# Performance work log

Hardware: AMD Instinct MI355X
Metric: run time of the kernel (lower is better)

The kernel has to match this reference:

```python
import jax, jax.numpy as jnp
import numpy as np

N = 40000        # nodes
E = 640000       # edges (avg degree 16)
D = 128          # in_dim = hidden_dim = out_dim (heads=1)
L = 3            # num_layers
BLOCK = 64       # big-bird local window
KEEP_P = 0.1     # probability an out-of-window edge is randomly kept
NEG = -1e9


def _xavier(key, shape):
    lim = np.sqrt(6.0 / (shape[-2] + shape[-1])).astype(np.float32)
    return jax.random.uniform(key, shape, jnp.float32, -lim, lim)


def setup_inputs() -> dict:
    key = jax.random.key(0)
    ks = jax.random.split(key, 11)
    x = jax.random.normal(ks[0], (N, D), jnp.float32)
    edge_index = jax.random.randint(ks[1], (2, E), 0, N, dtype=jnp.int64)
    # stacked per-layer params (all layers are D->D since heads=1)
    Wq = _xavier(ks[2], (L, D, D)); Wk = _xavier(ks[3], (L, D, D))
    Wv = _xavier(ks[4], (L, D, D)); Wo = _xavier(ks[5], (L, D, D))
    bq = jax.random.uniform(ks[6], (L, D), jnp.float32, -0.05, 0.05)
    bk = jax.random.uniform(ks[7], (L, D), jnp.float32, -0.05, 0.05)
    bv = jax.random.uniform(ks[8], (L, D), jnp.float32, -0.05, 0.05)
    bo = jax.random.uniform(ks[9], (L, D), jnp.float32, -0.05, 0.05)
    return {"x": x, "edge_index": edge_index,
            "Wq": Wq, "bq": bq, "Wk": Wk, "bk": bk,
            "Wv": Wv, "bv": bv, "Wo": Wo, "bo": bo}


def _bigbird_layer(h, src, dst, edge_mask, Wq, bq, Wk, bk, Wv, bv, Wo, bo):
    # h: [N, D]; src/dst: [E] int; edge_mask: [E] bool (True -> masked out)
    q = h @ Wq + bq                         # [N, D]
    k = h @ Wk + bk
    v = h @ Wv + bv
    scale = 1.0 / jnp.sqrt(jnp.asarray(D, h.dtype))
    alpha = jnp.sum(q[dst] * k[src], axis=-1) * scale   # [E] edge scores
    alpha = jnp.where(edge_mask, NEG, alpha)
    # segment softmax keyed by destination node
    m = jax.ops.segment_max(alpha, dst, num_segments=N)  # [N]
    e = jnp.exp(alpha - m[dst])                          # [E]
    s = jax.ops.segment_sum(e, dst, num_segments=N)      # [N]
    w = e / s[dst]                                       # [E]
    msg = v[src] * w[:, None]                            # [E, D]
    out = jax.ops.segment_sum(msg, dst, num_segments=N)  # [N, D]
    return out @ Wo + bo


def reference(x, edge_index, Wq, bq, Wk, bk, Wv, bv, Wo, bo):
    src, dst = edge_index[0], edge_index[1]
    local_mask = jnp.abs(src - dst) > BLOCK              # outside local window
    h = x
    for i in range(L):
        rkey = jax.random.fold_in(jax.random.key(42), i)
        rand_mask = jax.random.uniform(rkey, (E,)) > KEEP_P
        edge_mask = local_mask & rand_mask               # big-bird mask
        h = _bigbird_layer(h, src, dst, edge_mask,
                           Wq[i], bq[i], Wk[i], bk[i],
                           Wv[i], bv[i], Wo[i], bo[i])
        if i < L - 1:
            h = jax.nn.relu(h)  # dropout is identity in eval mode
    return h
```

## Files before the change

### kernel.cpp

```cpp
#include <hip/hip_runtime.h>
#include <hip/hip_bf16.h>
#include <stdint.h>
#include <math.h>

#define N_NODES 40000
#define N_EDGES 640000
#define DIM     128
#define NLAYERS 3
#define WINDOW  64
#define SCALE_F 0.08838834764831845f
#define CAP     96

#define CVT_XB   (N_NODES * DIM / 4 / 256)
#define CVT_BB   ((4 * NLAYERS * DIM + 255) / 256)
#define CVT_WB   (64 * 12)
#define CVT_CU   ((N_NODES + 255) / 256)
#define CVT_TOT  (CVT_XB + CVT_BB + CVT_WB + CVT_CU)

#define QKV_BLKS 1875
#define MASK_BLKS ((N_EDGES + 255) / 256)

#define HSTR 136

typedef unsigned int   u32;
typedef unsigned short u16;
typedef unsigned long long u64;
typedef unsigned char  u8;

typedef __attribute__((ext_vector_type(8))) short short8;
typedef __attribute__((ext_vector_type(4))) float f32x4;

__device__ inline float bf2f(u32 lo16) { return __uint_as_float(lo16 << 16); }
__device__ inline u16 f2bf(float f) {
  u32 x = __float_as_uint(f);
  u32 r = (x + 0x7fffu + ((x >> 16) & 1u)) >> 16;
  return (u16)r;
}

__host__ __device__ inline u32 rotl32(u32 v, int r) { return (v << r) | (v >> (32 - r)); }
#define TF_R4(a,b,c,d) \
  x0 += x1; x1 = rotl32(x1,a); x1 ^= x0; \
  x0 += x1; x1 = rotl32(x1,b); x1 ^= x0; \
  x0 += x1; x1 = rotl32(x1,c); x1 ^= x0; \
  x0 += x1; x1 = rotl32(x1,d); x1 ^= x0;

__host__ __device__ inline void tf2x32(u32 k0, u32 k1, u32 x0, u32 x1, u32& o0, u32& o1) {
  u32 ks2 = k0 ^ k1 ^ 0x1BD11BDAu;
  x0 += k0; x1 += k1;
  TF_R4(13,15,26,6);   x0 += k1;  x1 += ks2 + 1u;
  TF_R4(17,29,16,24);  x0 += ks2; x1 += k0  + 2u;
  TF_R4(13,15,26,6);   x0 += k0;  x1 += k1  + 3u;
  TF_R4(17,29,16,24);  x0 += k1;  x1 += ks2 + 4u;
  TF_R4(13,15,26,6);   x0 += ks2; x1 += k0  + 5u;
  o0 = x0; o1 = x1;
}

__device__ inline int ld_src(const int* ei, int e, int i64) {
  return i64 ? ei[2 * (size_t)e] : ei[e];
}
__device__ inline int ld_dst(const int* ei, int e, int i64) {
  return i64 ? ei[2 * ((size_t)N_EDGES + (size_t)e)] : ei[N_EDGES + e];
}

__device__ inline void detect_local(const u32* __restrict__ xw,
                                    const int* __restrict__ ei,
                                    int& fl, int& efl) {
  __shared__ int votes, nz;
  if (threadIdx.x == 0) { votes = 0; nz = 0; }
  __syncthreads();
  u32 w = xw[threadIdx.x * 777 + 13];
  int e = (w >> 7) & 0xFF;
  if (e < 100 || e > 135) atomicAdd(&votes, 1);
  if (ei[threadIdx.x * 5000 + 1] != 0) atomicAdd(&nz, 1);
  __syncthreads();
  fl  = (votes == 0) ? 1 : 0;
  efl = (nz == 0) ? 1 : 0;
}

__global__ void k_cvtall(const void* __restrict__ x, const int* __restrict__ ei,
                         const void* bq, const void* bk, const void* bv, const void* bo,
                         const void* Wq, const void* Wk, const void* Wv, const void* Wo,
                         int* __restrict__ flag, int* __restrict__ eflag,
                         int* __restrict__ cursor,
                         u16* __restrict__ xb, float* __restrict__ biasf,
                         u16* __restrict__ wswz) {
  int b = blockIdx.x;
  int fl, efl;
  detect_local((const u32*)x, ei, fl, efl);
  if (b == 0 && threadIdx.x == 0) { *flag = fl; *eflag = efl; }
  if (b < CVT_XB) {
    int i = b * 256 + threadIdx.x;
    if (fl) {
      ((u64*)xb)[i] = ((const u64*)x)[i];
    } else {
      f32x4 v = ((const f32x4*)x)[i];
      u64 p = (u64)f2bf(v.x) | ((u64)f2bf(v.y) << 16)
            | ((u64)f2bf(v.z) << 32) | ((u64)f2bf(v.w) << 48);
      ((u64*)xb)[i] = p;
    }
  } else if (b < CVT_XB + CVT_BB) {
    int i = (b - CVT_XB) * 256 + threadIdx.x;
    if (i < 4 * NLAYERS * DIM) {
      int which = i / (NLAYERS * DIM), rem = i % (NLAYERS * DIM);
      const void* src = (which == 0) ? bq : (which == 1) ? bk : (which == 2) ? bv : bo;
      biasf[i] = fl ? bf2f(((const u16*)src)[rem]) : ((const float*)src)[rem];
    }
  } else if (b < CVT_XB + CVT_BB + CVT_WB) {
    int bb = b - CVT_XB - CVT_BB;
    int m = bb >> 6;
    int l = m >> 2, t = m & 3;
    const void* base = (t == 0 ? Wq : t == 1 ? Wk : t == 2 ? Wv : Wo);
    int idx = (bb & 63) * 256 + threadIdx.x;
    int k = idx >> 7, n = idx & 127;
    u16 val;
    if (fl) val = ((const u16*)base)[l * DIM * DIM + idx];
    else    val = f2bf(((const float*)base)[l * DIM * DIM + idx]);
    int nf = n >> 4, col = n & 15, kk = k >> 5, hi = (k >> 3) & 3, j = k & 7;
    wswz[m * 16384 + ((nf * 4 + kk) * 64 + hi * 16 + col) * 8 + j] = val;
  } else {
    int i = (b - CVT_XB - CVT_BB - CVT_WB) * 256 + threadIdx.x;
    if (i < N_NODES) cursor[i] = 0;
  }
}

__device__ inline void gemm_frags(const u16* A, int rowBase, int lane, short8 af[4]) {
  const u16* arow = A + (size_t)(rowBase + (lane & 15)) * DIM;
  #pragma unroll
  for (int kk = 0; kk < 4; ++kk)
    af[kk] = *(const short8*)(arow + kk * 32 + (lane >> 4) * 8);
}

__global__ __launch_bounds__(256) void k_qkv0_mask(
    const u16* __restrict__ A, const u16* __restrict__ wswzL,
    const float* __restrict__ biasL,
    u16* __restrict__ qb, u16* __restrict__ kb, u16* __restrict__ vb,
    const int* __restrict__ ei, const int* __restrict__ eflag,
    u16* __restrict__ edst, u32* __restrict__ esrck,
    u32 ka0, u32 ka1, u32 kb0, u32 kb1, u32 kc0, u32 kc1) {
  int b = blockIdx.x;
  if (b < QKV_BLKS) {
    int z = b / 625, bx = b - z * 625;
    const u16* W = wswzL + z * 16384;
    const float* bias = biasL + z * NLAYERS * DIM;
    u16* out = (z == 0) ? qb : (z == 1) ? kb : vb;
    int tid = threadIdx.x, wave = tid >> 6, lane = tid & 63;
    int rowBase = bx * 64 + wave * 16;
    short8 af[4];
    gemm_frags(A, rowBase, lane, af);
    int col = lane & 15, rowOff = (lane >> 4) * 4;
    #pragma unroll
    for (int nf = 0; nf < 8; ++nf) {
      f32x4 acc = {0.f, 0.f, 0.f, 0.f};
      #pragma unroll
      for (int kk = 0; kk < 4; ++kk) {
        short8 bfm = *(const short8*)(W + ((nf * 4 + kk) * 64 + lane) * 8);
        acc = __builtin_amdgcn_mfma_f32_16x16x32_bf16(af[kk], bfm, acc, 0, 0, 0);
      }
      float bv = bias[nf * 16 + col];
      #pragma unroll
      for (int i = 0; i < 4; ++i) {
        float vv = acc[i] + bv;
        size_t oidx = (size_t)(rowBase + rowOff + i) * DIM + nf * 16 + col;
        out[oidx] = f2bf(vv);
      }
    }
  } else {
    int e = (b - QKV_BLKS) * 256 + threadIdx.x;
    if (e >= N_EDGES) return;
    int i64 = *eflag;
    int s = ld_src(ei, e, i64), d = ld_dst(ei, e, i64);
    bool loc = abs(s - d) <= WINDOW;
    u32 keys[6] = {ka0, ka1, kb0, kb1, kc0, kc1};
    u32 kept = 0;
    #pragma unroll
    for (int l = 0; l < 3; ++l) {
      u32 b1, b2;
      tf2x32(keys[2*l], keys[2*l+1], 0u, (u32)e, b1, b2);
      u32 bits = b1 ^ b2;
      float u = __uint_as_float(0x3f800000u | (bits >> 9)) - 1.0f;
      if (loc || (u <= 0.1f)) kept |= (1u << l);
    }
    edst[e]  = (u16)d;
    esrck[e] = (u32)s | (kept << 16);
  }
}

__global__ void k_scatter(const u16* __restrict__ edst, const u32* __restrict__ esrck,
                          int* __restrict__ cursor, u32* __restrict__ csr) {
  int c = blockIdx.x & 7;
  int e = (blockIdx.x >> 3) * 256 + threadIdx.x;
  if (e >= N_EDGES) return;
  int d = edst[e];
  if (((d >> 8) & 7) != c) return;
  u32 sk = esrck[e];
  int pos = atomicAdd(&cursor[d], 1);
  if (pos < CAP) csr[(size_t)d * CAP + pos] = sk;
}

__global__ void k_beacon(float* __restrict__ outf, const int* __restrict__ flag,
                         int ws_bad_mb) {
  if (threadIdx.x != 0 || blockIdx.x != 0) return;
  if (*flag == 1) outf[1] = 1024.0f;
  if (ws_bad_mb)  outf[2] = 4096.0f + (float)ws_bad_mb;
}

__global__ __launch_bounds__(256) void k_gemm_oqkv(
    const u16* __restrict__ A,
    const u16* __restrict__ Wo_swz, const float* __restrict__ bo_f,
    const u16* __restrict__ wswzN, const float* __restrict__ biasN,
    u16* __restrict__ qb, u16* __restrict__ kb, u16* __restrict__ vb) {
  __shared__ u16 hl[64 * HSTR];
  int z = blockIdx.z;
  int tid = threadIdx.x, wave = tid >> 6, lane = tid & 63;
  int rowBase = blockIdx.x * 64 + wave * 16;
  int col = lane & 15, rowOff = (lane >> 4) * 4;
  {
    short8 af[4];
    gemm_frags(A, rowBase, lane, af);
    #pragma unroll
    for (int nf = 0; nf < 8; ++nf) {
      f32x4 acc = {0.f, 0.f, 0.f, 0.f};
      #pragma unroll
      for (int kk = 0; kk < 4; ++kk) {
        short8 bfm = *(const short8*)(Wo_swz + ((nf * 4 + kk) * 64 + lane) * 8);
        acc = __builtin_amdgcn_mfma_f32_16x16x32_bf16(af[kk], bfm, acc, 0, 0, 0);
      }
      float bv = bo_f[nf * 16 + col];
      #pragma unroll
      for (int i = 0; i < 4; ++i) {
        float vv = fmaxf(acc[i] + bv, 0.f);
        hl[(wave * 16 + rowOff + i) * HSTR + nf * 16 + col] = f2bf(vv);
      }
    }
  }
  __syncthreads();
  const u16* W = wswzN + z * 16384;
  const float* bias = biasN + z * NLAYERS * DIM;
  u16* out = (z == 0) ? qb : (z == 1) ? kb : vb;
  short8 af2[4];
  {
    const u16* arow = hl + (size_t)(wave * 16 + (lane & 15)) * HSTR;
    #pragma unroll
    for (int kk = 0; kk < 4; ++kk)
      af2[kk] = *(const short8*)(arow + kk * 32 + (lane >> 4) * 8);
  }
  #pragma unroll
  for (int nf = 0; nf < 8; ++nf) {
    f32x4 acc = {0.f, 0.f, 0.f, 0.f};
    #pragma unroll
    for (int kk = 0; kk < 4; ++kk) {
      short8 bfm = *(const short8*)(W + ((nf * 4 + kk) * 64 + lane) * 8);
      acc = __builtin_amdgcn_mfma_f32_16x16x32_bf16(af2[kk], bfm, acc, 0, 0, 0);
    }
    float bv = bias[nf * 16 + col];
    #pragma unroll
    for (int i = 0; i < 4; ++i) {
      float vv = acc[i] + bv;
      size_t oidx = (size_t)(rowBase + rowOff + i) * DIM + nf * 16 + col;
      out[oidx] = f2bf(vv);
    }
  }
}

__global__ __launch_bounds__(256) void k_gemm_o(
    const u16* __restrict__ A, const u16* __restrict__ W,
    const float* __restrict__ bias,
    void* __restrict__ fout, const int* __restrict__ flag) {
  int tid = threadIdx.x, wave = tid >> 6, lane = tid & 63;
  int rowBase = blockIdx.x * 64 + wave * 16;
  short8 af[4];
  gemm_frags(A, rowBase, lane, af);
  int col = lane & 15, rowOff = (lane >> 4) * 4;
  int bf16out = *flag;
  #pragma unroll
  for (int nf = 0; nf < 8; ++nf) {
    f32x4 acc = {0.f, 0.f, 0.f, 0.f};
    #pragma unroll
    for (int kk = 0; kk < 4; ++kk) {
      short8 bfm = *(const short8*)(W + ((nf * 4 + kk) * 64 + lane) * 8);
      acc = __builtin_amdgcn_mfma_f32_16x16x32_bf16(af[kk], bfm, acc, 0, 0, 0);
    }
    float bv = bias[nf * 16 + col];
    #pragma unroll
    for (int i = 0; i < 4; ++i) {
      float vv = acc[i] + bv;
      size_t oidx = (size_t)(rowBase + rowOff + i) * DIM + nf * 16 + col;
      if (bf16out) ((u16*)fout)[oidx] = f2bf(vv);
      else         ((float*)fout)[oidx] = vv;
    }
  }
}

__global__ __launch_bounds__(256) void k_agg(
    const u16* __restrict__ qb, const u16* __restrict__ kb,
    const u16* __restrict__ vb,
    const int* __restrict__ cursor, const u32* __restrict__ csr,
    int layer, u16* __restrict__ msg) {
  int wid  = blockIdx.x * 4 + (threadIdx.x >> 6);
  int lane = threadIdx.x & 63;
  int deg = cursor[wid];
  if (deg > CAP) deg = CAP;
  size_t beg = (size_t)wid * CAP;
  const u32 keptbit = 1u << (16 + layer);
  float m = -__builtin_inff(), s = 0.f, a0 = 0.f, a1 = 0.f;

  if (deg <= 64) {
    u32 en = (lane < deg) ? csr[beg + lane] : 0u;
    u64 km = __ballot((lane < deg) && (en & keptbit));
    if (!km) {
      for (int base = 0; base < deg; base += 4) {
        int c = deg - base; if (c > 4) c = 4;
        u32 w0 = 0, w1 = 0, w2 = 0, w3 = 0;
        if (c > 0) { int t = __shfl((int)en, base + 0) & 0xffff;
                     w0 = ((const u32*)(vb + (size_t)t * DIM))[lane]; }
        if (c > 1) { int t = __shfl((int)en, base + 1) & 0xffff;
                     w1 = ((const u32*)(vb + (size_t)t * DIM))[lane]; }
        if (c > 2) { int t = __shfl((int)en, base + 2) & 0xffff;
                     w2 = ((const u32*)(vb + (size_t)t * DIM))[lane]; }
        if (c > 3) { int t = __shfl((int)en, base + 3) & 0xffff;
                     w3 = ((const u32*)(vb + (size_t)t * DIM))[lane]; }
        if (c > 0) { a0 += bf2f(w0 & 0xffffu); a1 += bf2f(w0 >> 16); }
        if (c > 1) { a0 += bf2f(w1 & 0xffffu); a1 += bf2f(w1 >> 16); }
        if (c > 2) { a0 += bf2f(w2 & 0xffffu); a1 += bf2f(w2 >> 16); }
        if (c > 3) { a0 += bf2f(w3 & 0xffffu); a1 += bf2f(w3 >> 16); }
      }
      s = (float)deg;
    } else if (!(km & (km - 1))) {
      int i = __ffsll((unsigned long long)km) - 1;
      int src = __shfl((int)en, i) & 0xffff;
      u32 vw = ((const u32*)(vb + (size_t)src * DIM))[lane];
      a0 = bf2f(vw & 0xffffu);
      a1 = bf2f(vw >> 16);
      s = 1.f;
    } else {
      u32 qw = ((const u32*)(qb + (size_t)wid * DIM))[lane];
      float q0 = bf2f(qw & 0xffffu), q1 = bf2f(qw >> 16);
      u64 rem = km;
      int i0 = __ffsll((unsigned long long)rem) - 1; rem &= rem - 1;
      int src0 = __shfl((int)en, i0) & 0xffff;
      u32 kw = ((const u32*)(kb + (size_t)src0 * DIM))[lane];
      u32 vw = ((const u32*)(vb + (size_t)src0 * DIM))[lane];
      while (1) {
        u32 kwc = kw, vwc = vw;
        bool more = (rem != 0);
        if (more) {
          int in = __ffsll((unsigned long long)rem) - 1; rem &= rem - 1;
          int sn = __shfl((int)en, in) & 0xffff;
          kw = ((const u32*)(kb + (size_t)sn * DIM))[lane];
          vw = ((const u32*)(vb + (size_t)sn * DIM))[lane];
        }
        float p = q0 * bf2f(kwc & 0xffffu) + q1 * bf2f(kwc >> 16);
        #pragma unroll
        for (int o = 32; o; o >>= 1) p += __shfl_xor(p, o, 64);
        float alpha = p * SCALE_F;
        float mn = fmaxf(m, alpha);
        float c  = __expf(m - mn);
        float w  = __expf(alpha - mn);
        s  = s * c + w;
        a0 = a0 * c + w * bf2f(vwc & 0xffffu);
        a1 = a1 * c + w * bf2f(vwc >> 16);
        m = mn;
        if (!more) break;
      }
    }
  } else {
    u32 qw = ((const u32*)(qb + (size_t)wid * DIM))[lane];
    float q0 = bf2f(qw & 0xffffu), q1 = bf2f(qw >> 16);
    bool anyKept = false;
    for (int base = 0; base < deg; base += 64) {
      int cnt = min(64, deg - base);
      u32 en = (lane < cnt) ? csr[beg + base + lane] : 0u;
      if (__ballot((lane < cnt) && (en & keptbit))) anyKept = true;
    }
    for (int base = 0; base < deg; base += 64) {
      int cnt = min(64, deg - base);
      u32 en = (lane < cnt) ? csr[beg + base + lane] : 0u;
      if (!anyKept) {
        for (int i = 0; i < cnt; ++i) {
          int src = __shfl((int)en, i) & 0xffff;
          u32 vw = ((const u32*)(vb + (size_t)src * DIM))[lane];
          a0 += bf2f(vw & 0xffffu);
          a1 += bf2f(vw >> 16);
        }
        s += (float)cnt;
      } else {
        u64 km = __ballot((lane < cnt) && (en & keptbit));
        while (km) {
          int i = __ffsll((unsigned long long)km) - 1;
          km &= km - 1;
          int src = __shfl((int)en, i) & 0xffff;
          u32 kw = ((const u32*)(kb + (size_t)src * DIM))[lane];
          u32 vw = ((const u32*)(vb + (size_t)src * DIM))[lane];
          float p = q0 * bf2f(kw & 0xffffu) + q1 * bf2f(kw >> 16);
          #pragma unroll
          for (int o = 32; o; o >>= 1) p += __shfl_xor(p, o, 64);
          float alpha = p * SCALE_F;
          float mn = fmaxf(m, alpha);
          float c  = __expf(m - mn);
          float w  = __expf(alpha - mn);
          s  = s * c + w;
          a0 = a0 * c + w * bf2f(vw & 0xffffu);
          a1 = a1 * c + w * bf2f(vw >> 16);
          m = mn;
        }
      }
    }
  }
  float inv = (s > 0.f) ? 1.f / s : 0.f;
  ((u32*)(msg + (size_t)wid * DIM))[lane] =
      (u32)f2bf(a0 * inv) | ((u32)f2bf(a1 * inv) << 16);
}

extern "C" void kernel_launch(void* const* d_in, const int* in_sizes, int n_in,
                              void* d_out, int out_size, void* d_ws, size_t ws_size,
                              hipStream_t stream) {
  const void* x  = d_in[0];
  const int*  ei = (const int*)d_in[1];
  const void* Wq = d_in[2];
  const void* bq = d_in[3];
  const void* Wk = d_in[4];
  const void* bk = d_in[5];
  const void* Wv = d_in[6];
  const void* bv = d_in[7];
  const void* Wo = d_in[8];
  const void* bo = d_in[9];

  char* ws = (char*)d_ws;
  size_t off = 0;
  auto alloc = [&](size_t bytes) -> void* {
    void* p = ws + off;
    off += (bytes + 255) & ~(size_t)255;
    return p;
  };
  u16*   xb   = (u16*)alloc((size_t)N_NODES * DIM * 2);
  u16*   qb   = (u16*)alloc((size_t)N_NODES * DIM * 2);
  u16*   kb2  = (u16*)alloc((size_t)N_NODES * DIM * 2);
  u16*   vb2  = (u16*)alloc((size_t)N_NODES * DIM * 2);
  u16*   msgb = (u16*)alloc((size_t)N_NODES * DIM * 2);
  u16*   edst  = (u16*)alloc((size_t)N_EDGES * 2);
  u32*   esrck = (u32*)alloc((size_t)N_EDGES * 4);
  int*   cursor    = (int*)alloc((size_t)N_NODES * 4);
  u32*   csr       = (u32*)alloc((size_t)N_NODES * CAP * 4);
  u16*   wswz      = (u16*)alloc((size_t)12 * 16384 * 2);
  float* biasf     = (float*)alloc((size_t)4 * NLAYERS * DIM * 4);
  int*   flag      = (int*)alloc(256);
  int*   eflag     = (int*)alloc(256);
  size_t needed = off;
  int ws_bad_mb = (ws_size < needed) ? (int)(ws_size >> 20) + 1 : 0;
  (void)in_sizes; (void)n_in; (void)out_size;

  u32 lk[6];
  for (int l = 0; l < 3; ++l) {
    u32 o0, o1;
    tf2x32(0u, 42u, 0u, (u32)l, o0, o1);
    lk[2 * l] = o0; lk[2 * l + 1] = o1;
  }

  k_cvtall<<<CVT_TOT, 256, 0, stream>>>(
      x, ei, bq, bk, bv, bo, Wq, Wk, Wv, Wo, flag, eflag, cursor, xb, biasf, wswz);
  k_qkv0_mask<<<QKV_BLKS + MASK_BLKS, 256, 0, stream>>>(
      xb, wswz, biasf, qb, kb2, vb2,
      ei, eflag, edst, esrck, lk[0], lk[1], lk[2], lk[3], lk[4], lk[5]);
  k_scatter<<<8 * ((N_EDGES + 255) / 256), 256, 0, stream>>>(edst, esrck, cursor, csr);

  k_agg<<<N_NODES / 4, 256, 0, stream>>>(qb, kb2, vb2, cursor, csr, 0, msgb);
  for (int l = 0; l < NLAYERS - 1; ++l) {
    k_gemm_oqkv<<<dim3(N_NODES / 64, 1, 3), 256, 0, stream>>>(
        msgb,
        wswz + (size_t)(l * 4 + 3) * 16384, biasf + (size_t)(3 * NLAYERS + l) * DIM,
        wswz + (size_t)((l + 1) * 4) * 16384, biasf + (size_t)(l + 1) * DIM,
        qb, kb2, vb2);
    k_agg<<<N_NODES / 4, 256, 0, stream>>>(qb, kb2, vb2, cursor, csr, l + 1, msgb);
  }
  k_gemm_o<<<N_NODES / 64, 256, 0, stream>>>(
      msgb, wswz + (size_t)(2 * 4 + 3) * 16384,
      biasf + (size_t)(3 * NLAYERS + 2) * DIM, d_out, flag);

  k_beacon<<<1, 64, 0, stream>>>((float*)d_out, flag, ws_bad_mb);
}
```

Measured before the change: 192.4 us.

## Batch four kept edges per online-softmax step and interleave q/k/v GEMM blocks

The multi-kept-edge path of the aggregation kernel now gathers up to four K/V rows at once, runs the four dot-product reductions interleaved, and folds them into the online softmax with a single rescale. This exposes more memory-level parallelism and cuts the serial shuffle-reduction chain. The q/k/v GEMM kernels also map block index to (z = b%3, row tile = b/3), so blocks that share the same A rows run next to each other, which should improve cache reuse of the activations. The cost is more registers in the aggregation kernel and different floating-point summation order.

```diff
diff --git a/kernel.cpp b/kernel.cpp
--- a/kernel.cpp
+++ b/kernel.cpp
@@ -10,6 +10,7 @@
 #define WINDOW  64
 #define SCALE_F 0.08838834764831845f
 #define CAP     96
+#define NEG_INF (-__builtin_inff())
 
 #define CVT_XB   (N_NODES * DIM / 4 / 256)
 #define CVT_BB   ((4 * NLAYERS * DIM + 255) / 256)
@@ -139,7 +140,7 @@
     u32 ka0, u32 ka1, u32 kb0, u32 kb1, u32 kc0, u32 kc1) {
   int b = blockIdx.x;
   if (b < QKV_BLKS) {
-    int z = b / 625, bx = b - z * 625;
+    int z = b % 3, bx = b / 3;
     const u16* W = wswzL + z * 16384;
     const float* bias = biasL + z * NLAYERS * DIM;
     u16* out = (z == 0) ? qb : (z == 1) ? kb : vb;
@@ -210,9 +211,10 @@
     const u16* __restrict__ wswzN, const float* __restrict__ biasN,
     u16* __restrict__ qb, u16* __restrict__ kb, u16* __restrict__ vb) {
   __shared__ u16 hl[64 * HSTR];
-  int z = blockIdx.z;
+  int b = blockIdx.x;
+  int z = b % 3, bx = b / 3;
   int tid = threadIdx.x, wave = tid >> 6, lane = tid & 63;
-  int rowBase = blockIdx.x * 64 + wave * 16;
+  int rowBase = bx * 64 + wave * 16;
   int col = lane & 15, rowOff = (lane >> 4) * 4;
   {
     short8 af[4];
@@ -302,7 +304,7 @@
   if (deg > CAP) deg = CAP;
   size_t beg = (size_t)wid * CAP;
   const u32 keptbit = 1u << (16 + layer);
-  float m = -__builtin_inff(), s = 0.f, a0 = 0.f, a1 = 0.f;
+  float m = NEG_INF, s = 0.f, a0 = 0.f, a1 = 0.f;
 
   if (deg <= 64) {
     u32 en = (lane < deg) ? csr[beg + lane] : 0u;
@@ -336,31 +338,55 @@
       u32 qw = ((const u32*)(qb + (size_t)wid * DIM))[lane];
       float q0 = bf2f(qw & 0xffffu), q1 = bf2f(qw >> 16);
       u64 rem = km;
-      int i0 = __ffsll((unsigned long long)rem) - 1; rem &= rem - 1;
-      int src0 = __shfl((int)en, i0) & 0xffff;
-      u32 kw = ((const u32*)(kb + (size_t)src0 * DIM))[lane];
-      u32 vw = ((const u32*)(vb + (size_t)src0 * DIM))[lane];
-      while (1) {
-        u32 kwc = kw, vwc = vw;
-        bool more = (rem != 0);
-        if (more) {
-          int in = __ffsll((unsigned long long)rem) - 1; rem &= rem - 1;
-          int sn = __shfl((int)en, in) & 0xffff;
-          kw = ((const u32*)(kb + (size_t)sn * DIM))[lane];
-          vw = ((const u32*)(vb + (size_t)sn * DIM))[lane];
+      while (rem) {
+        int n = 1;
+        int j0 = __ffsll((unsigned long long)rem) - 1; rem &= rem - 1;
+        int j1 = 0, j2 = 0, j3 = 0;
+        if (rem) { j1 = __ffsll((unsigned long long)rem) - 1; rem &= rem - 1; n = 2; }
+        if (rem) { j2 = __ffsll((unsigned long long)rem) - 1; rem &= rem - 1; n = 3; }
+        if (rem) { j3 = __ffsll((unsigned long long)rem) - 1; rem &= rem - 1; n = 4; }
+        u32 kw0 = 0, kw1 = 0, kw2 = 0, kw3 = 0;
+        u32 vw0 = 0, vw1 = 0, vw2 = 0, vw3 = 0;
+        {            int t = __shfl((int)en, j0) & 0xffff;
+                     kw0 = ((const u32*)(kb + (size_t)t * DIM))[lane];
+                     vw0 = ((const u32*)(vb + (size_t)t * DIM))[lane]; }
+        if (n > 1) { int t = __shfl((int)en, j1) & 0xffff;
+                     kw1 = ((const u32*)(kb + (size_t)t * DIM))[lane];
+                     vw1 = ((const u32*)(vb + (size_t)t * DIM))[lane]; }
+        if (n > 2) { int t = __shfl((int)en, j2) & 0xffff;
+                     kw2 = ((const u32*)(kb + (size_t)t * DIM))[lane];
+                     vw2 = ((const u32*)(vb + (size_t)t * DIM))[lane]; }
+        if (n > 3) { int t = __shfl((int)en, j3) & 0xffff;
+                     kw3 = ((const u32*)(kb + (size_t)t * DIM))[lane];
+                     vw3 = ((const u32*)(vb + (size_t)t * DIM))[lane]; }
+        float p0 = q0 * bf2f(kw0 & 0xffffu) + q1 * bf2f(kw0 >> 16);
+        float p1 = q0 * bf2f(kw1 & 0xffffu) + q1 * bf2f(kw1 >> 16);
+        float p2 = q0 * bf2f(kw2 & 0xffffu) + q1 * bf2f(kw2 >> 16);
+        float p3 = q0 * bf2f(kw3 & 0xffffu) + q1 * bf2f(kw3 >> 16);
+        #pragma unroll
+        for (int o = 32; o; o >>= 1) {
+          p0 += __shfl_xor(p0, o, 64);
+          p1 += __shfl_xor(p1, o, 64);
+          p2 += __shfl_xor(p2, o, 64);
+          p3 += __shfl_xor(p3, o, 64);
         }
-        float p = q0 * bf2f(kwc & 0xffffu) + q1 * bf2f(kwc >> 16);
-        #pragma unroll
-        for (int o = 32; o; o >>= 1) p += __shfl_xor(p, o, 64);
-        float alpha = p * SCALE_F;
-        float mn = fmaxf(m, alpha);
-        float c  = __expf(m - mn);
-        float w  = __expf(alpha - mn);
-        s  = s * c + w;
-        a0 = a0 * c + w * bf2f(vwc & 0xffffu);
-        a1 = a1 * c + w * bf2f(vwc >> 16);
+        float A0 = p0 * SCALE_F;
+        float A1 = (n > 1) ? p1 * SCALE_F : NEG_INF;
+        float A2 = (n > 2) ? p2 * SCALE_F : NEG_INF;
+        float A3 = (n > 3) ? p3 * SCALE_F : NEG_INF;
+        float mc = fmaxf(fmaxf(A0, A1), fmaxf(A2, A3));
+        float mn = fmaxf(m, mc);
+        float cc = __expf(m - mn);
+        float e0 = __expf(A0 - mn);
+        float e1 = __expf(A1 - mn);
+        float e2 = __expf(A2 - mn);
+        float e3 = __expf(A3 - mn);
+        s  = s * cc + ((e0 + e1) + (e2 + e3));
+        a0 = a0 * cc + (e0 * bf2f(vw0 & 0xffffu) + e1 * bf2f(vw1 & 0xffffu))
+                     + (e2 * bf2f(vw2 & 0xffffu) + e3 * bf2f(vw3 & 0xffffu));
+        a1 = a1 * cc + (e0 * bf2f(vw0 >> 16) + e1 * bf2f(vw1 >> 16))
+                     + (e2 * bf2f(vw2 >> 16) + e3 * bf2f(vw3 >> 16));
         m = mn;
-        if (!more) break;
       }
     }
   } else {
@@ -465,7 +491,7 @@
 
   k_agg<<<N_NODES / 4, 256, 0, stream>>>(qb, kb2, vb2, cursor, csr, 0, msgb);
   for (int l = 0; l < NLAYERS - 1; ++l) {
-    k_gemm_oqkv<<<dim3(N_NODES / 64, 1, 3), 256, 0, stream>>>(
+    k_gemm_oqkv<<<QKV_BLKS, 256, 0, stream>>>(
         msgb,
         wswz + (size_t)(l * 4 + 3) * 16384, biasf + (size_t)(3 * NLAYERS + l) * DIM,
         wswz + (size_t)((l + 1) * 4) * 16384, biasf + (size_t)(l + 1) * DIM,
```

Measured after the change: 191.2 us. About the same (-0.6%).
